# Optimization experiments

Hardware: AMD Instinct MI355X
Metric: run time of the kernel (lower is better)

Reference implementation:

```python
import jax, jax.numpy as jnp
import numpy as np

B, N, D = 8, 2048, 1024
LAM = 0.7
EPS = 1e-8

def setup_inputs() -> dict:
    key = jax.random.key(0)
    k1, k2, k3, k4, k5 = jax.random.split(key, 5)
    scale = 1.0 / np.sqrt(D)
    return {
        "node_states": jax.random.normal(k1, (B, N, D), jnp.float32),
        "node_gates": jax.random.uniform(k2, (B, N, 1), jnp.float32),
        "r_acc": jax.random.normal(k3, (B, N, N), jnp.float32),
        "W_in": jax.random.normal(k4, (D, D), jnp.float32) * scale,
        "W_out": jax.random.normal(k5, (D, D), jnp.float32) * scale,
        "conductance": jnp.float32(1.0),
    }

def _phase_resonance(a):
    # a: (B, N, D) -> resonance (B, N, N).
    # cos(ta - tb) mean over pairs == (cos@cos^T + sin@sin^T)/pairs (exact identity)
    b_, n_, d_ = a.shape
    pairs = d_ // 2
    x2 = a.reshape(b_, n_, pairs, 2)
    theta = jnp.arctan2(x2[..., 1] + EPS, x2[..., 0] + EPS)  # (B,N,pairs)
    ca, sa = jnp.cos(theta), jnp.sin(theta)
    r = jnp.einsum('bnp,bmp->bnm', ca, ca) + jnp.einsum('bnp,bmp->bnm', sa, sa)
    return r / pairs

def reference(node_states, node_gates, r_acc, W_in, W_out, conductance):
    b_, n_, d_ = node_states.shape
    transmitted = node_states * node_gates                     # (B,N,D)
    a = node_states @ W_in.T                                   # field_in (B,N,D)
    r_instant = _phase_resonance(a)                            # (B,N,N)
    r_acc_new = jnp.clip(LAM * r_acc + (1.0 - LAM) * r_instant, -2.0, 2.0)
    cond = jnp.clip(conductance, -5.0, 5.0)
    coupling = jax.nn.sigmoid(cond * r_acc_new)                # (B,N,N)
    eye = jnp.eye(n_, dtype=coupling.dtype)[None]              # zero self-coupling
    coupling = coupling * (1.0 - eye)
    coupling = coupling * jnp.swapaxes(node_gates, -1, -2)     # gate senders (B,1,N)
    coupling = coupling * node_gates                           # gate receivers (B,N,1)
    coupling = coupling / (coupling.sum(axis=-1, keepdims=True) + 1e-8)
    values = transmitted @ W_out.T                             # (B,N,D)
    field_signal = coupling @ values                           # (B,N,D)
    return field_signal, r_acc_new
```

## Files before the change

kernel.cpp:

```cpp
#include <hip/hip_runtime.h>
#include <cstdint>

#define B_ 8
#define N_ 2048
#define D_ 1024

typedef __attribute__((ext_vector_type(8))) short bf16x8;
typedef __attribute__((ext_vector_type(4))) float f32x4;

__device__ __forceinline__ ushort f2bf(float f) {
  union { float f; uint32_t u; } v; v.f = f;
  return (ushort)((v.u + 0x7fffu + ((v.u >> 16) & 1u)) >> 16);
}

__device__ __forceinline__ void gload_lds16(const void* g, void* l) {
  __builtin_amdgcn_global_load_lds(
      (const __attribute__((address_space(1))) void*)(uintptr_t)g,
      (__attribute__((address_space(3))) void*)(uint32_t)(uintptr_t)l,
      16, 0, 0);
}

__device__ __forceinline__ void stage_tile(const ushort* g, int ldg, ushort* lds, int tid) {
  int wave = tid >> 6, lane = tid & 63;
  const ushort* gp = g + (size_t)(wave * 8 + (lane >> 3)) * ldg + ((lane & 7) * 8);
  ushort* lp = lds + wave * 512;
#pragma unroll
  for (int q = 0; q < 4; ++q) {
    gload_lds16(gp, lp);
    gp += (size_t)32 * ldg;
    lp += 2048;
  }
}

struct GParams {
  const ushort* A; const ushort* B;
  long sAz, sBz;
  int lda, ldb, K;
  ushort* u_out;
  const float* gates;
  ushort* vT_out;
  const float* r_in;
  float* r_out;
  ushort* c_out;
  float* S;
  const float* condp;
  float* field;
};

template<int MODE>
__global__ __launch_bounds__(256, 2)
void gemm_nt(GParams p) {
  __shared__ __align__(16) ushort sA[128 * 64];
  __shared__ __align__(16) ushort sB[128 * 64];
  int tid = threadIdx.x;
  int z = blockIdx.z;
  const ushort* Ab = p.A + (size_t)z * p.sAz + (size_t)blockIdx.y * 128 * p.lda;
  const ushort* Bb = p.B + (size_t)z * p.sBz + (size_t)blockIdx.x * 128 * p.ldb;

  f32x4 acc[4][4];
#pragma unroll
  for (int i = 0; i < 4; ++i)
#pragma unroll
    for (int j = 0; j < 4; ++j) acc[i][j] = (f32x4)0.f;

  int lane = tid & 63, wid = tid >> 6;
  int wm = wid >> 1, wn = wid & 1, quad = lane >> 4, tn = lane & 15;

  for (int k0 = 0; k0 < p.K; k0 += 64) {
    stage_tile(Ab + k0, p.lda, sA, tid);
    stage_tile(Bb + k0, p.ldb, sB, tid);
    __syncthreads();
#pragma unroll
    for (int kk = 0; kk < 64; kk += 32) {
      bf16x8 av[4], bv[4];
#pragma unroll
      for (int t = 0; t < 4; ++t) {
        av[t] = *(const bf16x8*)(sA + (wm * 64 + t * 16 + tn) * 64 + kk + quad * 8);
        bv[t] = *(const bf16x8*)(sB + (wn * 64 + t * 16 + tn) * 64 + kk + quad * 8);
      }
#pragma unroll
      for (int i = 0; i < 4; ++i)
#pragma unroll
        for (int j = 0; j < 4; ++j)
          acc[i][j] = __builtin_amdgcn_mfma_f32_16x16x32_bf16(av[i], bv[j], acc[i][j], 0, 0, 0);
    }
    __syncthreads();
  }

  int row0 = blockIdx.y * 128 + wm * 64 + quad * 4;
  int col0 = blockIdx.x * 128 + wn * 64 + tn;

  if constexpr (MODE == 0) {
    bool even = (tn & 1) == 0;
#pragma unroll
    for (int i = 0; i < 4; ++i) {
      int rbase = row0 + i * 16;
#pragma unroll
      for (int j = 0; j < 4; ++j) {
        int col = col0 + j * 16;
        int pp = col >> 1;
        int d = even ? pp : 512 + pp;
#pragma unroll
        for (int r = 0; r < 4; ++r) {
          float v = acc[i][j][r];
          float w = __shfl_xor(v, 1);
          float xe = (even ? v : w) + 1e-8f;
          float ye = (even ? w : v) + 1e-8f;
          float rinv = rsqrtf(xe * xe + ye * ye);
          float val = (even ? xe : ye) * rinv;
          p.u_out[(size_t)(rbase + r) * 1024 + d] = f2bf(val);
        }
      }
    }
  } else if constexpr (MODE == 1) {
#pragma unroll
    for (int i = 0; i < 4; ++i) {
      int rbase = row0 + i * 16;
      float g0 = p.gates[rbase + 0];
      float g1 = p.gates[rbase + 1];
      float g2 = p.gates[rbase + 2];
      float g3 = p.gates[rbase + 3];
      int b = rbase >> 11;
      int nloc = rbase & 2047;
#pragma unroll
      for (int j = 0; j < 4; ++j) {
        int d = col0 + j * 16;
        ushort4 pk;
        pk.x = f2bf(acc[i][j][0] * g0);
        pk.y = f2bf(acc[i][j][1] * g1);
        pk.z = f2bf(acc[i][j][2] * g2);
        pk.w = f2bf(acc[i][j][3] * g3);
        *(ushort4*)(p.vT_out + ((size_t)b * 1024 + d) * 2048 + nloc) = pk;
      }
    }
  } else if constexpr (MODE == 2) {
    float cond = p.condp[0];
    cond = fminf(5.f, fmaxf(-5.f, cond));
    const float* g = p.gates + (size_t)z * 2048;
    float rs[4][4];
#pragma unroll
    for (int i = 0; i < 4; ++i)
#pragma unroll
      for (int r = 0; r < 4; ++r) rs[i][r] = 0.f;
#pragma unroll
    for (int i = 0; i < 4; ++i) {
      int nb = row0 + i * 16;
#pragma unroll
      for (int j = 0; j < 4; ++j) {
        int m = col0 + j * 16;
        float gm = g[m];
#pragma unroll
        for (int r = 0; r < 4; ++r) {
          int n = nb + r;
          size_t idx = ((size_t)z * 2048 + n) * 2048 + m;
          float rinst = acc[i][j][r] * (1.0f / 512.0f);
          float rnew = 0.7f * p.r_in[idx] + 0.3f * rinst;
          rnew = fminf(2.f, fmaxf(-2.f, rnew));
          p.r_out[idx] = rnew;
          float cv = 0.f;
          if (m != n) cv = gm * g[n] / (1.f + __expf(-cond * rnew));
          p.c_out[idx] = f2bf(cv);
          rs[i][r] += cv;
        }
      }
    }
#pragma unroll
    for (int i = 0; i < 4; ++i)
#pragma unroll
      for (int r = 0; r < 4; ++r) {
        float s = rs[i][r];
        s += __shfl_xor(s, 1);
        s += __shfl_xor(s, 2);
        s += __shfl_xor(s, 4);
        s += __shfl_xor(s, 8);
        if (tn == 0) atomicAdd(p.S + (size_t)z * 2048 + row0 + i * 16 + r, s);
      }
  } else {
#pragma unroll
    for (int i = 0; i < 4; ++i) {
      int nb = row0 + i * 16;
      float sc[4];
#pragma unroll
      for (int r = 0; r < 4; ++r) sc[r] = 1.f / (p.S[(size_t)z * 2048 + nb + r] + 1e-8f);
#pragma unroll
      for (int j = 0; j < 4; ++j) {
        int d = col0 + j * 16;
#pragma unroll
        for (int r = 0; r < 4; ++r)
          p.field[((size_t)z * 2048 + nb + r) * 1024 + d] = acc[i][j][r] * sc[r];
      }
    }
  }
}

__global__ void cvt_bf16(const float* __restrict__ src, ushort* __restrict__ dst, int n4) {
  int i = blockIdx.x * blockDim.x + threadIdx.x;
  if (i < n4) {
    float4 f = ((const float4*)src)[i];
    ushort4 o;
    o.x = f2bf(f.x); o.y = f2bf(f.y); o.z = f2bf(f.z); o.w = f2bf(f.w);
    ((ushort4*)dst)[i] = o;
  }
}

extern "C" void kernel_launch(void* const* d_in, const int* in_sizes, int n_in,
                              void* d_out, int out_size, void* d_ws, size_t ws_size,
                              hipStream_t stream) {
  const float* states = (const float*)d_in[0];
  const float* gates  = (const float*)d_in[1];
  const float* r_acc  = (const float*)d_in[2];
  const float* W_in   = (const float*)d_in[3];
  const float* W_out  = (const float*)d_in[4];
  const float* condp  = (const float*)d_in[5];

  float* field = (float*)d_out;
  float* r_out = field + (size_t)B_ * N_ * D_;

  char* w = (char*)d_ws;
  ushort* Xb  = (ushort*)w; w += (size_t)B_ * N_ * D_ * 2;
  ushort* Wib = (ushort*)w; w += (size_t)D_ * D_ * 2;
  ushort* Wob = (ushort*)w; w += (size_t)D_ * D_ * 2;
  ushort* U   = (ushort*)w; w += (size_t)B_ * N_ * D_ * 2;
  ushort* VT  = (ushort*)w; w += (size_t)B_ * D_ * N_ * 2;
  ushort* C   = (ushort*)w; w += (size_t)B_ * N_ * N_ * 2;
  float*  S   = (float*)w;

  hipMemsetAsync(S, 0, (size_t)B_ * N_ * 4, stream);

  cvt_bf16<<<dim3(B_ * N_ * D_ / 4 / 256), 256, 0, stream>>>(states, Xb, B_ * N_ * D_ / 4);
  cvt_bf16<<<dim3(D_ * D_ / 4 / 256), 256, 0, stream>>>(W_in, Wib, D_ * D_ / 4);
  cvt_bf16<<<dim3(D_ * D_ / 4 / 256), 256, 0, stream>>>(W_out, Wob, D_ * D_ / 4);

  GParams p0{};
  p0.A = Xb; p0.B = Wib; p0.sAz = 0; p0.sBz = 0;
  p0.lda = D_; p0.ldb = D_; p0.K = D_;
  p0.u_out = U;
  gemm_nt<0><<<dim3(8, 128, 1), 256, 0, stream>>>(p0);

  GParams p1{};
  p1.A = Xb; p1.B = Wob; p1.sAz = 0; p1.sBz = 0;
  p1.lda = D_; p1.ldb = D_; p1.K = D_;
  p1.gates = gates; p1.vT_out = VT;
  gemm_nt<1><<<dim3(8, 128, 1), 256, 0, stream>>>(p1);

  GParams p2{};
  p2.A = U; p2.B = U; p2.sAz = (long)N_ * D_; p2.sBz = (long)N_ * D_;
  p2.lda = D_; p2.ldb = D_; p2.K = D_;
  p2.gates = gates; p2.r_in = r_acc; p2.r_out = r_out;
  p2.c_out = C; p2.S = S; p2.condp = condp;
  gemm_nt<2><<<dim3(16, 16, 8), 256, 0, stream>>>(p2);

  GParams p3{};
  p3.A = C; p3.B = VT; p3.sAz = (long)N_ * N_; p3.sBz = (long)D_ * N_;
  p3.lda = N_; p3.ldb = N_; p3.K = N_;
  p3.S = S; p3.field = field;
  gemm_nt<3><<<dim3(8, 16, 8), 256, 0, stream>>>(p3);
}
```

Baseline: 793.9 us.

## Transpose MFMA accumulator fragments in-register to vectorize epilogue memory accesses

```diff
diff --git a/kernel.cpp b/kernel.cpp
--- a/kernel.cpp
+++ b/kernel.cpp
@@ -30,6 +30,17 @@
     gp += (size_t)32 * ldg;
     lp += 2048;
   }
+}
+
+__device__ __forceinline__ void quad_transpose(float v[4], int s) {
+  float x0 = __shfl_xor((s & 1) ? v[0] : v[1], 1);
+  if (s & 1) v[0] = x0; else v[1] = x0;
+  float x1 = __shfl_xor((s & 1) ? v[2] : v[3], 1);
+  if (s & 1) v[2] = x1; else v[3] = x1;
+  float y0 = __shfl_xor((s & 2) ? v[0] : v[2], 2);
+  if (s & 2) v[0] = y0; else v[2] = y0;
+  float y1 = __shfl_xor((s & 2) ? v[1] : v[3], 2);
+  if (s & 2) v[1] = y1; else v[3] = y1;
 }
 
 struct GParams {
@@ -48,7 +59,7 @@
 };
 
 template<int MODE>
-__global__ __launch_bounds__(256, 2)
+__global__ __launch_bounds__(256, 4)
 void gemm_nt(GParams p) {
   __shared__ __align__(16) ushort sA[128 * 64];
   __shared__ __align__(16) ushort sB[128 * 64];
@@ -88,28 +99,27 @@
   }
 
   int row0 = blockIdx.y * 128 + wm * 64 + quad * 4;
-  int col0 = blockIdx.x * 128 + wn * 64 + tn;
+  int colbase = blockIdx.x * 128 + wn * 64;
+  int s = tn & 3, t4 = tn & 12;
 
   if constexpr (MODE == 0) {
-    bool even = (tn & 1) == 0;
-#pragma unroll
-    for (int i = 0; i < 4; ++i) {
-      int rbase = row0 + i * 16;
-#pragma unroll
-      for (int j = 0; j < 4; ++j) {
-        int col = col0 + j * 16;
-        int pp = col >> 1;
-        int d = even ? pp : 512 + pp;
-#pragma unroll
-        for (int r = 0; r < 4; ++r) {
-          float v = acc[i][j][r];
-          float w = __shfl_xor(v, 1);
-          float xe = (even ? v : w) + 1e-8f;
-          float ye = (even ? w : v) + 1e-8f;
-          float rinv = rsqrtf(xe * xe + ye * ye);
-          float val = (even ? xe : ye) * rinv;
-          p.u_out[(size_t)(rbase + r) * 1024 + d] = f2bf(val);
-        }
+#pragma unroll
+    for (int i = 0; i < 4; ++i) {
+      int n = row0 + i * 16 + s;
+#pragma unroll
+      for (int j = 0; j < 4; ++j) {
+        float v[4] = {acc[i][j][0], acc[i][j][1], acc[i][j][2], acc[i][j][3]};
+        quad_transpose(v, s);
+        int c0 = colbase + j * 16 + t4;
+        float xe0 = v[0] + 1e-8f, ye0 = v[1] + 1e-8f;
+        float xe1 = v[2] + 1e-8f, ye1 = v[3] + 1e-8f;
+        float ri0 = rsqrtf(xe0 * xe0 + ye0 * ye0);
+        float ri1 = rsqrtf(xe1 * xe1 + ye1 * ye1);
+        int pp = c0 >> 1;
+        ushort2 ca; ca.x = f2bf(xe0 * ri0); ca.y = f2bf(xe1 * ri1);
+        ushort2 sa; sa.x = f2bf(ye0 * ri0); sa.y = f2bf(ye1 * ri1);
+        *(ushort2*)(p.u_out + (size_t)n * 1024 + pp) = ca;
+        *(ushort2*)(p.u_out + (size_t)n * 1024 + 512 + pp) = sa;
       }
     }
   } else if constexpr (MODE == 1) {
@@ -124,7 +134,7 @@
       int nloc = rbase & 2047;
 #pragma unroll
       for (int j = 0; j < 4; ++j) {
-        int d = col0 + j * 16;
+        int d = colbase + j * 16 + tn;
         ushort4 pk;
         pk.x = f2bf(acc[i][j][0] * g0);
         pk.y = f2bf(acc[i][j][1] * g1);
@@ -137,57 +147,58 @@
     float cond = p.condp[0];
     cond = fminf(5.f, fmaxf(-5.f, cond));
     const float* g = p.gates + (size_t)z * 2048;
-    float rs[4][4];
-#pragma unroll
-    for (int i = 0; i < 4; ++i)
-#pragma unroll
-      for (int r = 0; r < 4; ++r) rs[i][r] = 0.f;
-#pragma unroll
-    for (int i = 0; i < 4; ++i) {
-      int nb = row0 + i * 16;
-#pragma unroll
-      for (int j = 0; j < 4; ++j) {
-        int m = col0 + j * 16;
-        float gm = g[m];
-#pragma unroll
-        for (int r = 0; r < 4; ++r) {
-          int n = nb + r;
-          size_t idx = ((size_t)z * 2048 + n) * 2048 + m;
-          float rinst = acc[i][j][r] * (1.0f / 512.0f);
-          float rnew = 0.7f * p.r_in[idx] + 0.3f * rinst;
-          rnew = fminf(2.f, fmaxf(-2.f, rnew));
-          p.r_out[idx] = rnew;
-          float cv = 0.f;
-          if (m != n) cv = gm * g[n] / (1.f + __expf(-cond * rnew));
-          p.c_out[idx] = f2bf(cv);
-          rs[i][r] += cv;
-        }
-      }
-    }
-#pragma unroll
-    for (int i = 0; i < 4; ++i)
-#pragma unroll
-      for (int r = 0; r < 4; ++r) {
-        float s = rs[i][r];
-        s += __shfl_xor(s, 1);
-        s += __shfl_xor(s, 2);
-        s += __shfl_xor(s, 4);
-        s += __shfl_xor(s, 8);
-        if (tn == 0) atomicAdd(p.S + (size_t)z * 2048 + row0 + i * 16 + r, s);
-      }
+    float rs[4];
+#pragma unroll
+    for (int i = 0; i < 4; ++i) rs[i] = 0.f;
+#pragma unroll
+    for (int i = 0; i < 4; ++i) {
+      int n = row0 + i * 16 + s;
+      float gn = g[n];
+#pragma unroll
+      for (int j = 0; j < 4; ++j) {
+        float v[4] = {acc[i][j][0], acc[i][j][1], acc[i][j][2], acc[i][j][3]};
+        quad_transpose(v, s);
+        int m0 = colbase + j * 16 + t4;
+        size_t idx = ((size_t)z * 2048 + n) * 2048 + m0;
+        float4 rin = *(const float4*)(p.r_in + idx);
+        float4 gm = *(const float4*)(g + m0);
+        float4 ro;
+        ro.x = fminf(2.f, fmaxf(-2.f, 0.7f * rin.x + v[0] * (0.3f / 512.0f)));
+        ro.y = fminf(2.f, fmaxf(-2.f, 0.7f * rin.y + v[1] * (0.3f / 512.0f)));
+        ro.z = fminf(2.f, fmaxf(-2.f, 0.7f * rin.z + v[2] * (0.3f / 512.0f)));
+        ro.w = fminf(2.f, fmaxf(-2.f, 0.7f * rin.w + v[3] * (0.3f / 512.0f)));
+        *(float4*)(p.r_out + idx) = ro;
+        float cv0 = (m0 + 0 != n) ? gn * gm.x / (1.f + __expf(-cond * ro.x)) : 0.f;
+        float cv1 = (m0 + 1 != n) ? gn * gm.y / (1.f + __expf(-cond * ro.y)) : 0.f;
+        float cv2 = (m0 + 2 != n) ? gn * gm.z / (1.f + __expf(-cond * ro.z)) : 0.f;
+        float cv3 = (m0 + 3 != n) ? gn * gm.w / (1.f + __expf(-cond * ro.w)) : 0.f;
+        ushort4 cpk;
+        cpk.x = f2bf(cv0); cpk.y = f2bf(cv1); cpk.z = f2bf(cv2); cpk.w = f2bf(cv3);
+        *(ushort4*)(p.c_out + idx) = cpk;
+        rs[i] += cv0 + cv1 + cv2 + cv3;
+      }
+    }
+#pragma unroll
+    for (int i = 0; i < 4; ++i) {
+      float sum = rs[i];
+      sum += __shfl_xor(sum, 4);
+      sum += __shfl_xor(sum, 8);
+      if (t4 == 0)
+        atomicAdd(p.S + (size_t)z * 2048 + row0 + i * 16 + s, sum);
+    }
   } else {
 #pragma unroll
     for (int i = 0; i < 4; ++i) {
-      int nb = row0 + i * 16;
-      float sc[4];
-#pragma unroll
-      for (int r = 0; r < 4; ++r) sc[r] = 1.f / (p.S[(size_t)z * 2048 + nb + r] + 1e-8f);
-#pragma unroll
-      for (int j = 0; j < 4; ++j) {
-        int d = col0 + j * 16;
-#pragma unroll
-        for (int r = 0; r < 4; ++r)
-          p.field[((size_t)z * 2048 + nb + r) * 1024 + d] = acc[i][j][r] * sc[r];
+      int n = row0 + i * 16 + s;
+      float sc = 1.f / (p.S[(size_t)z * 2048 + n] + 1e-8f);
+#pragma unroll
+      for (int j = 0; j < 4; ++j) {
+        float v[4] = {acc[i][j][0], acc[i][j][1], acc[i][j][2], acc[i][j][3]};
+        quad_transpose(v, s);
+        int d0 = colbase + j * 16 + t4;
+        float4 o;
+        o.x = v[0] * sc; o.y = v[1] * sc; o.z = v[2] * sc; o.w = v[3] * sc;
+        *(float4*)(p.field + ((size_t)z * 2048 + n) * 1024 + d0) = o;
       }
     }
   }
```

New measurement: 653.6 us. -17.7%, faster.
